# Kernel optimization log

Measured on AMD Instinct MI355X. Metric: run time of the kernel, lower is better.

Reference implementation:

```python
import jax, jax.numpy as jnp
import numpy as np

N_NEWS, N_ENT, N_TOP = 100000, 50000, 2000
D = 128
N_EDGES = 1600000
HID, OUT = 512, 128


def setup_inputs() -> dict:
    key = jax.random.key(0)
    ks = jax.random.split(key, 12)
    return {
        "news_feats": jax.random.normal(ks[0], (N_NEWS, D), jnp.float32),
        "entity_feats": jax.random.normal(ks[1], (N_ENT, D), jnp.float32),
        "topic_feats": jax.random.normal(ks[2], (N_TOP, D), jnp.float32),
        "ent_row": jax.random.randint(ks[3], (N_EDGES,), 0, N_NEWS, jnp.int32),
        "ent_col": jax.random.randint(ks[4], (N_EDGES,), 0, N_ENT, jnp.int32),
        "top_row": jax.random.randint(ks[5], (N_EDGES,), 0, N_NEWS, jnp.int32),
        "top_col": jax.random.randint(ks[6], (N_EDGES,), 0, N_TOP, jnp.int32),
        "W1": jax.random.normal(ks[7], (3 * D, HID), jnp.float32) * 0.05,
        "b1": jnp.zeros((HID,), jnp.float32),
        "W2": jax.random.normal(ks[8], (HID, OUT), jnp.float32) * 0.05,
        "b2": jnp.zeros((OUT,), jnp.float32),
    }


def _agg(feats, row, col, num_news):
    # SpMM with binary adjacency: sum neighbor feats per news node
    gathered = feats[col]                                   # [E, D]
    summed = jax.ops.segment_sum(gathered, row, num_segments=num_news)
    deg = jax.ops.segment_sum(jnp.ones_like(row, dtype=feats.dtype), row,
                              num_segments=num_news)
    return summed / (deg[:, None] + 1e-8)


def reference(news_feats, entity_feats, topic_feats, ent_row, ent_col,
              top_row, top_col, W1, b1, W2, b2):
    n = news_feats.shape[0]
    ent_agg = _agg(entity_feats, ent_row, ent_col, n)
    top_agg = _agg(topic_feats, top_row, top_col, n)
    out = jnp.concatenate([news_feats, ent_agg, top_agg], axis=1)  # [N, 3D]
    h = jnp.tanh(out @ W1 + b1)
    return h @ W2 + b2
```

## Files before the change

### kernel.cpp

```cpp
#include <hip/hip_runtime.h>
#include <hip/hip_bf16.h>

#define NN 100000
#define NE 50000
#define NT 2000
#define DD 128
#define NEDGE 1600000
#define HID 512
#define OUTD 128
#define K1 (3*DD)
#define NBKT 391

typedef __bf16 bf16x8 __attribute__((ext_vector_type(8)));
typedef __bf16 bf16x4 __attribute__((ext_vector_type(4)));
typedef float  f32x4  __attribute__((ext_vector_type(4)));

__device__ __forceinline__ __bf16 f2b(float f) {
    __hip_bfloat16 h = __float2bfloat16(f);
    union { __hip_bfloat16 h; __bf16 b; } u; u.h = h; return u.b;
}

__device__ __forceinline__ void gll16(const void* g, void* l) {
    __builtin_amdgcn_global_load_lds((const __attribute__((address_space(1))) void*)g,
                                     (__attribute__((address_space(3))) void*)l, 16, 0, 0);
}

__device__ __forceinline__ float ftanh(float x) {
    x = fminf(fmaxf(x, -15.f), 15.f);
    float t = __expf(2.f * x);
    return (t - 1.f) / (t + 1.f);
}

__global__ void conv_feats(const float* __restrict__ entf, const float* __restrict__ topf,
                           const float* __restrict__ news,
                           __bf16* __restrict__ entb, __bf16* __restrict__ topb,
                           __bf16* __restrict__ X) {
    long i = ((long)blockIdx.x * 256 + threadIdx.x) * 4;
    const long NEL = (long)NE * DD;
    const long NTL = (long)NT * DD;
    if (i < NEL) {
        float4 v = *(const float4*)(entf + i);
        *(bf16x4*)(entb + i) = bf16x4{f2b(v.x), f2b(v.y), f2b(v.z), f2b(v.w)};
    } else if (i < NEL + NTL) {
        long j = i - NEL;
        float4 v = *(const float4*)(topf + j);
        *(bf16x4*)(topb + j) = bf16x4{f2b(v.x), f2b(v.y), f2b(v.z), f2b(v.w)};
    } else {
        long j = i - NEL - NTL;
        long row = j >> 7, col = j & 127;
        float4 v = *(const float4*)(news + j);
        *(bf16x4*)(X + row * K1 + col) = bf16x4{f2b(v.x), f2b(v.y), f2b(v.z), f2b(v.w)};
    }
}

__global__ __launch_bounds__(256) void hist_buckets(const int* __restrict__ er,
                                                    const int* __restrict__ tr,
                                                    int* __restrict__ bc_e,
                                                    int* __restrict__ bc_t) {
    __shared__ int lhe[NBKT], lht[NBKT];
    const int tid = threadIdx.x;
    for (int i = tid; i < NBKT; i += 256) { lhe[i] = 0; lht[i] = 0; }
    __syncthreads();
    const int base = blockIdx.x * 8192;
    #pragma unroll 4
    for (int k = 0; k < 32; k++) {
        int e = base + k * 256 + tid;
        if (e < NEDGE) {
            atomicAdd(&lhe[er[e] >> 8], 1);
            atomicAdd(&lht[tr[e] >> 8], 1);
        }
    }
    __syncthreads();
    for (int i = tid; i < NBKT; i += 256) {
        if (lhe[i]) atomicAdd(&bc_e[i], lhe[i]);
        if (lht[i]) atomicAdd(&bc_t[i], lht[i]);
    }
}

__global__ void scan_buckets(int* __restrict__ bc_e, int* __restrict__ bc_t,
                             int* __restrict__ cur_e, int* __restrict__ cur_t,
                             int* __restrict__ offs_e, int* __restrict__ offs_t) {
    int* bc  = blockIdx.y ? bc_t : bc_e;
    int* cur = blockIdx.y ? cur_t : cur_e;
    int* offs = blockIdx.y ? offs_t : offs_e;
    __shared__ int s[512];
    int i = threadIdx.x;
    s[i] = (i < NBKT) ? bc[i] : 0;
    __syncthreads();
    #pragma unroll
    for (int off = 1; off < 512; off <<= 1) {
        int v = (i >= off) ? s[i - off] : 0;
        __syncthreads();
        s[i] += v;
        __syncthreads();
    }
    if (i < NBKT) {
        bc[i] = s[i];
        cur[i] = i ? s[i - 1] : 0;
    }
    if (i == 0) offs[0] = 0;
}

__global__ __launch_bounds__(256) void scatter_bucket(const int* __restrict__ er,
                                                      const int* __restrict__ ec,
                                                      const int* __restrict__ tr,
                                                      const int* __restrict__ tc,
                                                      int* __restrict__ cur_e,
                                                      int* __restrict__ cur_t,
                                                      int* __restrict__ be,
                                                      int* __restrict__ bt) {
    __shared__ int lhe[NBKT], lht[NBKT];
    __shared__ int lbe[NBKT], lbt[NBKT];
    const int tid = threadIdx.x;
    for (int i = tid; i < NBKT; i += 256) { lhe[i] = 0; lht[i] = 0; }
    __syncthreads();
    const int base = blockIdx.x * 4096;
    #pragma unroll 4
    for (int k = 0; k < 16; k++) {
        int e = base + k * 256 + tid;
        if (e < NEDGE) {
            atomicAdd(&lhe[er[e] >> 8], 1);
            atomicAdd(&lht[tr[e] >> 8], 1);
        }
    }
    __syncthreads();
    for (int i = tid; i < NBKT; i += 256) {
        int c = lhe[i];
        lbe[i] = c ? atomicAdd(&cur_e[i], c) : 0;
        lhe[i] = 0;
        c = lht[i];
        lbt[i] = c ? atomicAdd(&cur_t[i], c) : 0;
        lht[i] = 0;
    }
    __syncthreads();
    #pragma unroll 4
    for (int k = 0; k < 16; k++) {
        int e = base + k * 256 + tid;
        if (e < NEDGE) {
            int r = er[e];
            int b = r >> 8;
            int p = lbe[b] + atomicAdd(&lhe[b], 1);
            be[p] = ((r & 255) << 16) | ec[e];
            r = tr[e];
            b = r >> 8;
            p = lbt[b] + atomicAdd(&lht[b], 1);
            bt[p] = ((r & 255) << 16) | tc[e];
        }
    }
}

__global__ __launch_bounds__(256) void bucket_csr(const int* __restrict__ be,
                                                  const int* __restrict__ bt,
                                                  const int* __restrict__ bc_e,
                                                  const int* __restrict__ bc_t,
                                                  int* __restrict__ offs_e,
                                                  int* __restrict__ offs_t,
                                                  int* __restrict__ se,
                                                  int* __restrict__ st) {
    const int* buf = blockIdx.y ? bt : be;
    const int* bc  = blockIdx.y ? bc_t : bc_e;
    int* offs      = blockIdx.y ? offs_t : offs_e;
    int* sout      = blockIdx.y ? st : se;
    const int b = blockIdx.x;
    const int tid = threadIdx.x;
    const int start = b ? bc[b - 1] : 0;
    const int cnt = bc[b] - start;

    __shared__ int scn[256];
    __shared__ int lcur[256];
    scn[tid] = 0;
    __syncthreads();
    for (int i = tid; i < cnt; i += 256)
        atomicAdd(&scn[buf[start + i] >> 16], 1);
    __syncthreads();
    #pragma unroll
    for (int off = 1; off < 256; off <<= 1) {
        int v = (tid >= off) ? scn[tid - off] : 0;
        __syncthreads();
        scn[tid] += v;
        __syncthreads();
    }
    const int node = b * 256 + tid;
    if (node < NN) offs[node + 1] = start + scn[tid];
    lcur[tid] = start + (tid ? scn[tid - 1] : 0);
    __syncthreads();
    for (int i = tid; i < cnt; i += 256) {
        int v = buf[start + i];
        int p = atomicAdd(&lcur[v >> 16], 1);
        sout[p] = v & 0xFFFF;
    }
}

__global__ __launch_bounds__(256) void aggregate2(const __bf16* __restrict__ entb,
                                                  const __bf16* __restrict__ topb,
                                                  const int* __restrict__ offs_e,
                                                  const int* __restrict__ offs_t,
                                                  const int* __restrict__ se,
                                                  const int* __restrict__ st,
                                                  __bf16* __restrict__ X) {
    const int wave = threadIdx.x >> 6, lane = threadIdx.x & 63;
    const int node = blockIdx.x * 4 + wave;
    if (node >= NN) return;
    const int h = lane >> 4;
    const int d = (lane & 15) * 8;

    float ea[8] = {0,0,0,0,0,0,0,0};
    float pa[8] = {0,0,0,0,0,0,0,0};

    const int s0 = offs_e[node], s1 = offs_e[node + 1];
    int i = s0 + h;
    for (; i + 12 < s1; i += 16) {
        int c0 = se[i], c1 = se[i + 4], c2 = se[i + 8], c3 = se[i + 12];
        bf16x8 v0 = *(const bf16x8*)(entb + (long)c0 * DD + d);
        bf16x8 v1 = *(const bf16x8*)(entb + (long)c1 * DD + d);
        bf16x8 v2 = *(const bf16x8*)(entb + (long)c2 * DD + d);
        bf16x8 v3 = *(const bf16x8*)(entb + (long)c3 * DD + d);
        #pragma unroll
        for (int j = 0; j < 8; j++)
            ea[j] += ((float)v0[j] + (float)v1[j]) + ((float)v2[j] + (float)v3[j]);
    }
    for (; i < s1; i += 4) {
        bf16x8 v = *(const bf16x8*)(entb + (long)se[i] * DD + d);
        #pragma unroll
        for (int j = 0; j < 8; j++) ea[j] += (float)v[j];
    }

    const int t0 = offs_t[node], t1 = offs_t[node + 1];
    i = t0 + h;
    for (; i + 12 < t1; i += 16) {
        int c0 = st[i], c1 = st[i + 4], c2 = st[i + 8], c3 = st[i + 12];
        bf16x8 v0 = *(const bf16x8*)(topb + (long)c0 * DD + d);
        bf16x8 v1 = *(const bf16x8*)(topb + (long)c1 * DD + d);
        bf16x8 v2 = *(const bf16x8*)(topb + (long)c2 * DD + d);
        bf16x8 v3 = *(const bf16x8*)(topb + (long)c3 * DD + d);
        #pragma unroll
        for (int j = 0; j < 8; j++)
            pa[j] += ((float)v0[j] + (float)v1[j]) + ((float)v2[j] + (float)v3[j]);
    }
    for (; i < t1; i += 4) {
        bf16x8 v = *(const bf16x8*)(topb + (long)st[i] * DD + d);
        #pragma unroll
        for (int j = 0; j < 8; j++) pa[j] += (float)v[j];
    }

    #pragma unroll
    for (int j = 0; j < 8; j++) {
        ea[j] += __shfl_xor(ea[j], 16, 64);
        ea[j] += __shfl_xor(ea[j], 32, 64);
        pa[j] += __shfl_xor(pa[j], 16, 64);
        pa[j] += __shfl_xor(pa[j], 32, 64);
    }

    const float ie = 1.0f / ((float)(s1 - s0) + 1e-8f);
    const float it = 1.0f / ((float)(t1 - t0) + 1e-8f);
    __bf16* xr = X + (long)node * K1;
    if (h == 1) {
        *(bf16x8*)(xr + DD + d) = bf16x8{f2b(ea[0]*ie), f2b(ea[1]*ie), f2b(ea[2]*ie), f2b(ea[3]*ie),
                                         f2b(ea[4]*ie), f2b(ea[5]*ie), f2b(ea[6]*ie), f2b(ea[7]*ie)};
    } else if (h == 2) {
        *(bf16x8*)(xr + 2*DD + d) = bf16x8{f2b(pa[0]*it), f2b(pa[1]*it), f2b(pa[2]*it), f2b(pa[3]*it),
                                           f2b(pa[4]*it), f2b(pa[5]*it), f2b(pa[6]*it), f2b(pa[7]*it)};
    }
}

__global__ void conv_w(const float* __restrict__ W1, const float* __restrict__ W2,
                       __bf16* __restrict__ W1T, __bf16* __restrict__ W2T) {
    int i = blockIdx.x * 256 + threadIdx.x;
    if (i < K1 * HID) {
        int k = i / HID, n = i % HID;
        W1T[n * K1 + k] = f2b(W1[i]);
    } else {
        int j = i - K1 * HID;
        if (j < HID * OUTD) {
            int k = j / OUTD, n = j % OUTD;
            W2T[n * HID + k] = f2b(W2[j]);
        }
    }
}


__device__ __forceinline__ void stage_tile(const __bf16* __restrict__ src, int ldK,
                                           int k0, int row0, int rowmax,
                                           __bf16* lds, int w, int lane) {
    #pragma unroll
    for (int half = 0; half < 2; half++) {
        int ss = w * 64 + half * 256 + lane;
        int r = ss >> 2;
        int sw = (r & 3) ^ ((r >> 2) & 3);
        int c = (ss & 3) ^ sw;
        int gr = row0 + r; if (gr >= rowmax) gr = rowmax - 1;
        gll16(src + (long)gr * ldK + k0 + c * 8,
              lds + (w * 64 + half * 256) * 8);
    }
}

__device__ __forceinline__ bf16x8 frag(const __bf16* lds, int r, int q) {
    int sw = (r & 3) ^ ((r >> 2) & 3);
    return *(const bf16x8*)(lds + (r * 4 + (q ^ sw)) * 8);
}

__device__ __forceinline__ void hs_write(__bf16* Hs, int r, int c, __bf16 v) {
    int ch = c >> 3;
    int pch = ((((ch >> 2) ^ ((r >> 2) & 3)) << 2) | ((ch & 3) ^ (r & 3)));
    Hs[(r * 16 + pch) * 8 + (c & 7)] = v;
}
__device__ __forceinline__ bf16x8 hs_frag(const __bf16* Hs, int r, int kk, int q) {
    int pch = (((kk ^ ((r >> 2) & 3)) << 2) | (q ^ (r & 3)));
    return *(const bf16x8*)(Hs + (r * 16 + pch) * 8);
}

__global__ __launch_bounds__(256, 2) void mlp_fused(const __bf16* __restrict__ X,
                                                    const __bf16* __restrict__ W1T,
                                                    const float* __restrict__ b1,
                                                    const __bf16* __restrict__ W2T,
                                                    const float* __restrict__ b2,
                                                    float* __restrict__ out) {
    __shared__ __bf16 Xs[2][128 * 32];
    __shared__ __bf16 Ws[2][128 * 32];
    __shared__ __bf16 Hs[128 * 128];
    const int bm = blockIdx.x * 128;
    const int t = threadIdx.x;
    const int lane = t & 63;
    const int w = t >> 6;
    const int quad = lane >> 4;
    const int l16 = lane & 15;
    const int wm = w >> 1, wn = w & 1;

    f32x4 oacc[4][4];
    #pragma unroll
    for (int i = 0; i < 4; i++)
        #pragma unroll
        for (int j = 0; j < 4; j++)
            #pragma unroll
            for (int r = 0; r < 4; r++) oacc[i][j][r] = 0.0f;

    stage_tile(X,   K1, 0, bm, NN,  Xs[0], w, lane);
    stage_tile(W1T, K1, 0, 0,  HID, Ws[0], w, lane);
    int cur = 0;
    __syncthreads();

    for (int nc = 0; nc < 4; nc++) {
        f32x4 hacc[4][4];
        #pragma unroll
        for (int i = 0; i < 4; i++)
            #pragma unroll
            for (int j = 0; j < 4; j++)
                #pragma unroll
                for (int r = 0; r < 4; r++) hacc[i][j][r] = 0.0f;

        for (int kt = 0; kt < 12; kt++) {
            const int nb = cur ^ 1;
            if (kt < 11) {
                stage_tile(X,   K1, (kt + 1) * 32, bm,       NN,  Xs[nb], w, lane);
                stage_tile(W1T, K1, (kt + 1) * 32, nc * 128, HID, Ws[nb], w, lane);
            } else {
                stage_tile(W2T, HID, nc * 128, 0, OUTD, Ws[nb], w, lane);
            }
            bf16x8 af[4], bfr[4];
            #pragma unroll
            for (int i = 0; i < 4; i++) {
                af[i]  = frag(Xs[cur], wm * 64 + i * 16 + l16, quad);
                bfr[i] = frag(Ws[cur], wn * 64 + i * 16 + l16, quad);
            }
            __builtin_amdgcn_s_setprio(1);
            #pragma unroll
            for (int i = 0; i < 4; i++)
                #pragma unroll
                for (int j = 0; j < 4; j++)
                    hacc[i][j] = __builtin_amdgcn_mfma_f32_16x16x32_bf16(af[i], bfr[j], hacc[i][j], 0, 0, 0);
            __builtin_amdgcn_s_setprio(0);
            __syncthreads();
            cur = nb;
        }

        #pragma unroll
        for (int j = 0; j < 4; j++) {
            const int col = wn * 64 + j * 16 + l16;
            const float bb = b1[nc * 128 + col];
            #pragma unroll
            for (int i = 0; i < 4; i++) {
                const int rbase = wm * 64 + i * 16 + quad * 4;
                #pragma unroll
                for (int r = 0; r < 4; r++)
                    hs_write(Hs, rbase + r, col, f2b(ftanh(hacc[i][j][r] + bb)));
            }
        }
        __syncthreads();

        for (int kk = 0; kk < 4; kk++) {
            const int nb = cur ^ 1;
            if (kk < 3) {
                stage_tile(W2T, HID, nc * 128 + (kk + 1) * 32, 0, OUTD, Ws[nb], w, lane);
            } else if (nc < 3) {
                stage_tile(X,   K1, 0, bm,             NN,  Xs[nb], w, lane);
                stage_tile(W1T, K1, 0, (nc + 1) * 128, HID, Ws[nb], w, lane);
            }
            bf16x8 af[4], bfr[4];
            #pragma unroll
            for (int i = 0; i < 4; i++) {
                af[i]  = hs_frag(Hs, wm * 64 + i * 16 + l16, kk, quad);
                bfr[i] = frag(Ws[cur], wn * 64 + i * 16 + l16, quad);
            }
            __builtin_amdgcn_s_setprio(1);
            #pragma unroll
            for (int i = 0; i < 4; i++)
                #pragma unroll
                for (int j = 0; j < 4; j++)
                    oacc[i][j] = __builtin_amdgcn_mfma_f32_16x16x32_bf16(af[i], bfr[j], oacc[i][j], 0, 0, 0);
            __builtin_amdgcn_s_setprio(0);
            __syncthreads();
            cur = nb;
        }
    }

    float bb[4];
    #pragma unroll
    for (int j = 0; j < 4; j++) bb[j] = b2[wn * 64 + j * 16 + l16];
    #pragma unroll
    for (int i = 0; i < 4; i++) {
        #pragma unroll
        for (int r = 0; r < 4; r++) {
            const int gr = bm + wm * 64 + i * 16 + quad * 4 + r;
            if (gr < NN) {
                float* orow = out + (long)gr * OUTD + wn * 64 + l16;
                #pragma unroll
                for (int j = 0; j < 4; j++)
                    orow[j * 16] = oacc[i][j][r] + bb[j];
            }
        }
    }
}

extern "C" void kernel_launch(void* const* d_in, const int* in_sizes, int n_in,
                              void* d_out, int out_size, void* d_ws, size_t ws_size,
                              hipStream_t stream) {
    const float* news  = (const float*)d_in[0];
    const float* ent_f = (const float*)d_in[1];
    const float* top_f = (const float*)d_in[2];
    const int* ent_row = (const int*)d_in[3];
    const int* ent_col = (const int*)d_in[4];
    const int* top_row = (const int*)d_in[5];
    const int* top_col = (const int*)d_in[6];
    const float* W1 = (const float*)d_in[7];
    const float* b1 = (const float*)d_in[8];
    const float* W2 = (const float*)d_in[9];
    const float* b2 = (const float*)d_in[10];

    char* ws = (char*)d_ws;
    int* offs_e = (int*)(ws + 0);
    int* offs_t = (int*)(ws + 400016);
    int* bc_e   = (int*)(ws + 800032);
    int* bc_t   = (int*)(ws + 801596);
    int* cur_e  = (int*)(ws + 803160);
    int* cur_t  = (int*)(ws + 804724);
    int* be     = (int*)(ws + 806320);
    int* bt     = (int*)(ws + 7206320);
    int* se     = (int*)(ws + 13606320);
    int* st     = (int*)(ws + 20006320);
    __bf16* entb = (__bf16*)(ws + 26406336);
    __bf16* topb = (__bf16*)(ws + 39206336);
    __bf16* X   = (__bf16*)(ws + 102400000);
    __bf16* W1T = (__bf16*)(ws + 179200000);
    __bf16* W2T = (__bf16*)(ws + 179593216);

    hipMemsetAsync(ws + 800032, 0, 6256, stream);
    conv_w<<<1024, 256, 0, stream>>>(W1, W2, W1T, W2T);
    conv_feats<<<19000, 256, 0, stream>>>(ent_f, top_f, news, entb, topb, X);
    hist_buckets<<<196, 256, 0, stream>>>(ent_row, top_row, bc_e, bc_t);
    scan_buckets<<<dim3(1, 2), 512, 0, stream>>>(bc_e, bc_t, cur_e, cur_t, offs_e, offs_t);
    scatter_bucket<<<392, 256, 0, stream>>>(ent_row, ent_col, top_row, top_col,
                                            cur_e, cur_t, be, bt);
    bucket_csr<<<dim3(NBKT, 2), 256, 0, stream>>>(be, bt, bc_e, bc_t,
                                                  offs_e, offs_t, se, st);
    aggregate2<<<NN / 4, 256, 0, stream>>>(entb, topb, offs_e, offs_t, se, st, X);
    mlp_fused<<<782, 256, 0, stream>>>(X, W1T, b1, W2T, b2, (float*)d_out);
}
```

Before: 540.4 us.

## Triple-buffer LDS staging in fused MLP with vmcnt-based waits

Moves the fused MLP kernel from double-buffered to triple-buffered LDS tiles for X and W1. Loads are now issued two k-steps ahead, and explicit s_waitcnt vmcnt plus s_barrier replace the per-iteration __syncthreads. The W2 staging in the second GEMM ping-pongs between the spare third buffers, so the next chunk's first X/W1 tiles can be prefetched during the second GEMM. The goal is to hide global-load latency, at the cost of more LDS (which may cut occupancy below 2 blocks per CU) and fragile hand-counted vmcnt values.

New measurement: 528.2 us. 1.02x faster.

```diff
diff --git a/kernel.cpp b/kernel.cpp
--- a/kernel.cpp
+++ b/kernel.cpp
@@ -315,8 +315,8 @@
                                                     const __bf16* __restrict__ W2T,
                                                     const float* __restrict__ b2,
                                                     float* __restrict__ out) {
-    __shared__ __bf16 Xs[2][128 * 32];
-    __shared__ __bf16 Ws[2][128 * 32];
+    __shared__ __bf16 Xs[3][128 * 32];
+    __shared__ __bf16 Ws[3][128 * 32];
     __shared__ __bf16 Hs[128 * 128];
     const int bm = blockIdx.x * 128;
     const int t = threadIdx.x;
@@ -334,10 +334,10 @@
             #pragma unroll
             for (int r = 0; r < 4; r++) oacc[i][j][r] = 0.0f;
 
-    stage_tile(X,   K1, 0, bm, NN,  Xs[0], w, lane);
-    stage_tile(W1T, K1, 0, 0,  HID, Ws[0], w, lane);
-    int cur = 0;
-    __syncthreads();
+    stage_tile(X,   K1, 0,  bm, NN,  Xs[0], w, lane);
+    stage_tile(W1T, K1, 0,  0,  HID, Ws[0], w, lane);
+    stage_tile(X,   K1, 32, bm, NN,  Xs[1], w, lane);
+    stage_tile(W1T, K1, 32, 0,  HID, Ws[1], w, lane);
 
     for (int nc = 0; nc < 4; nc++) {
         f32x4 hacc[4][4];
@@ -348,19 +348,22 @@
                 #pragma unroll
                 for (int r = 0; r < 4; r++) hacc[i][j][r] = 0.0f;
 
+        #pragma unroll
         for (int kt = 0; kt < 12; kt++) {
-            const int nb = cur ^ 1;
-            if (kt < 11) {
-                stage_tile(X,   K1, (kt + 1) * 32, bm,       NN,  Xs[nb], w, lane);
-                stage_tile(W1T, K1, (kt + 1) * 32, nc * 128, HID, Ws[nb], w, lane);
-            } else {
-                stage_tile(W2T, HID, nc * 128, 0, OUTD, Ws[nb], w, lane);
-            }
+            const int cb = kt % 3;
+            if (kt < 11) asm volatile("s_waitcnt vmcnt(4)" ::: "memory");
+            else         asm volatile("s_waitcnt vmcnt(0)" ::: "memory");
+            __builtin_amdgcn_s_barrier();
             bf16x8 af[4], bfr[4];
             #pragma unroll
             for (int i = 0; i < 4; i++) {
-                af[i]  = frag(Xs[cur], wm * 64 + i * 16 + l16, quad);
-                bfr[i] = frag(Ws[cur], wn * 64 + i * 16 + l16, quad);
+                af[i]  = frag(Xs[cb], wm * 64 + i * 16 + l16, quad);
+                bfr[i] = frag(Ws[cb], wn * 64 + i * 16 + l16, quad);
+            }
+            if (kt < 10) {
+                const int nb = (kt + 2) % 3;
+                stage_tile(X,   K1, (kt + 2) * 32, bm,       NN,  Xs[nb], w, lane);
+                stage_tile(W1T, K1, (kt + 2) * 32, nc * 128, HID, Ws[nb], w, lane);
             }
             __builtin_amdgcn_s_setprio(1);
             #pragma unroll
@@ -369,9 +372,10 @@
                 for (int j = 0; j < 4; j++)
                     hacc[i][j] = __builtin_amdgcn_mfma_f32_16x16x32_bf16(af[i], bfr[j], hacc[i][j], 0, 0, 0);
             __builtin_amdgcn_s_setprio(0);
-            __syncthreads();
-            cur = nb;
-        }
+        }
+        __syncthreads();
+
+        stage_tile(W2T, HID, nc * 128, 0, OUTD, Ws[2], w, lane);
 
         #pragma unroll
         for (int j = 0; j < 4; j++) {
@@ -388,18 +392,24 @@
         __syncthreads();
 
         for (int kk = 0; kk < 4; kk++) {
-            const int nb = cur ^ 1;
-            if (kk < 3) {
-                stage_tile(W2T, HID, nc * 128 + (kk + 1) * 32, 0, OUTD, Ws[nb], w, lane);
-            } else if (nc < 3) {
-                stage_tile(X,   K1, 0, bm,             NN,  Xs[nb], w, lane);
-                stage_tile(W1T, K1, 0, (nc + 1) * 128, HID, Ws[nb], w, lane);
+            __bf16* curb = (kk & 1) ? Xs[2] : Ws[2];
+            __bf16* nxtb = (kk & 1) ? Ws[2] : Xs[2];
+            if (kk < 3)
+                stage_tile(W2T, HID, nc * 128 + (kk + 1) * 32, 0, OUTD, nxtb, w, lane);
+            if (nc < 3) {
+                if (kk == 2) {
+                    stage_tile(X,   K1, 0, bm,             NN,  Xs[0], w, lane);
+                    stage_tile(W1T, K1, 0, (nc + 1) * 128, HID, Ws[0], w, lane);
+                } else if (kk == 3) {
+                    stage_tile(X,   K1, 32, bm,             NN,  Xs[1], w, lane);
+                    stage_tile(W1T, K1, 32, (nc + 1) * 128, HID, Ws[1], w, lane);
+                }
             }
             bf16x8 af[4], bfr[4];
             #pragma unroll
             for (int i = 0; i < 4; i++) {
                 af[i]  = hs_frag(Hs, wm * 64 + i * 16 + l16, kk, quad);
-                bfr[i] = frag(Ws[cur], wn * 64 + i * 16 + l16, quad);
+                bfr[i] = frag(curb, wn * 64 + i * 16 + l16, quad);
             }
             __builtin_amdgcn_s_setprio(1);
             #pragma unroll
@@ -409,7 +419,6 @@
                     oacc[i][j] = __builtin_amdgcn_mfma_f32_16x16x32_bf16(af[i], bfr[j], oacc[i][j], 0, 0, 0);
             __builtin_amdgcn_s_setprio(0);
             __syncthreads();
-            cur = nb;
         }
     }
 
```

## Keep full X tile resident in LDS and triple-buffer weights with vmcnt-based pipelining

Applied to the files above, without the earlier changes.

The fused MLP kernel now stages the whole 128x384 X tile into LDS once, so the first hidden chunk loads it and the later chunks reuse it instead of reloading X from global memory. Weight tiles go through a 3-slot ring with prefetch two phases ahead, and the loop syncs with explicit vmcnt waits plus a single barrier instead of __syncthreads double-buffering. Bias values are also preloaded into registers. The larger LDS footprint (about 152KB) lowers occupancy to one block per CU, which reduces latency hiding across blocks.

New measurement: 536.0 us. Within noise of the previous version (-0.8%).

```diff
diff --git a/kernel.cpp b/kernel.cpp
--- a/kernel.cpp
+++ b/kernel.cpp
@@ -309,14 +309,29 @@
     return *(const bf16x8*)(Hs + (r * 16 + pch) * 8);
 }
 
-__global__ __launch_bounds__(256, 2) void mlp_fused(const __bf16* __restrict__ X,
+__device__ __forceinline__ void stage_for_phase(int g, int bm,
+        const __bf16* __restrict__ X, const __bf16* __restrict__ W1T,
+        const __bf16* __restrict__ W2T,
+        __bf16* Xs, __bf16* Wst, int w, int lane) {
+    if (g >= 64) return;
+    const int ncg = g >> 4, ph = g & 15;
+    __bf16* wb = Wst + (g % 3) * 4096;
+    if (ph < 12) {
+        if (ncg == 0) stage_tile(X, K1, ph * 32, bm, NN, Xs + ph * 4096, w, lane);
+        stage_tile(W1T, K1, ph * 32, ncg * 128, HID, wb, w, lane);
+    } else {
+        stage_tile(W2T, HID, ncg * 128 + (ph - 12) * 32, 0, OUTD, wb, w, lane);
+    }
+}
+
+__global__ __launch_bounds__(256, 1) void mlp_fused(const __bf16* __restrict__ X,
                                                     const __bf16* __restrict__ W1T,
                                                     const float* __restrict__ b1,
                                                     const __bf16* __restrict__ W2T,
                                                     const float* __restrict__ b2,
                                                     float* __restrict__ out) {
-    __shared__ __bf16 Xs[2][128 * 32];
-    __shared__ __bf16 Ws[2][128 * 32];
+    __shared__ __bf16 Xs[12 * 4096];
+    __shared__ __bf16 Wst[3 * 4096];
     __shared__ __bf16 Hs[128 * 128];
     const int bm = blockIdx.x * 128;
     const int t = threadIdx.x;
@@ -326,6 +341,16 @@
     const int l16 = lane & 15;
     const int wm = w >> 1, wn = w & 1;
 
+    float b1r[4][4], b2r[4];
+    #pragma unroll
+    for (int nc = 0; nc < 4; nc++)
+        #pragma unroll
+        for (int j = 0; j < 4; j++)
+            b1r[nc][j] = b1[nc * 128 + wn * 64 + j * 16 + l16];
+    #pragma unroll
+    for (int j = 0; j < 4; j++) b2r[j] = b2[wn * 64 + j * 16 + l16];
+    asm volatile("s_waitcnt vmcnt(0)" ::: "memory");
+
     f32x4 oacc[4][4];
     #pragma unroll
     for (int i = 0; i < 4; i++)
@@ -334,10 +359,8 @@
             #pragma unroll
             for (int r = 0; r < 4; r++) oacc[i][j][r] = 0.0f;
 
-    stage_tile(X,   K1, 0, bm, NN,  Xs[0], w, lane);
-    stage_tile(W1T, K1, 0, 0,  HID, Ws[0], w, lane);
-    int cur = 0;
-    __syncthreads();
+    stage_for_phase(0, bm, X, W1T, W2T, Xs, Wst, w, lane);
+    stage_for_phase(1, bm, X, W1T, W2T, Xs, Wst, w, lane);
 
     for (int nc = 0; nc < 4; nc++) {
         f32x4 hacc[4][4];
@@ -348,20 +371,20 @@
                 #pragma unroll
                 for (int r = 0; r < 4; r++) hacc[i][j][r] = 0.0f;
 
+        #pragma unroll
         for (int kt = 0; kt < 12; kt++) {
-            const int nb = cur ^ 1;
-            if (kt < 11) {
-                stage_tile(X,   K1, (kt + 1) * 32, bm,       NN,  Xs[nb], w, lane);
-                stage_tile(W1T, K1, (kt + 1) * 32, nc * 128, HID, Ws[nb], w, lane);
-            } else {
-                stage_tile(W2T, HID, nc * 128, 0, OUTD, Ws[nb], w, lane);
+            if (nc == 0 && kt <= 10) asm volatile("s_waitcnt vmcnt(4)" ::: "memory");
+            else                     asm volatile("s_waitcnt vmcnt(2)" ::: "memory");
+            __builtin_amdgcn_s_barrier();
+            const __bf16* xb = Xs + kt * 4096;
+            const __bf16* wb = Wst + ((nc * 16 + kt) % 3) * 4096;
+            bf16x8 af[4], bfr[4];
+            #pragma unroll
+            for (int i = 0; i < 4; i++) {
+                af[i]  = frag(xb, wm * 64 + i * 16 + l16, quad);
+                bfr[i] = frag(wb, wn * 64 + i * 16 + l16, quad);
             }
-            bf16x8 af[4], bfr[4];
-            #pragma unroll
-            for (int i = 0; i < 4; i++) {
-                af[i]  = frag(Xs[cur], wm * 64 + i * 16 + l16, quad);
-                bfr[i] = frag(Ws[cur], wn * 64 + i * 16 + l16, quad);
-            }
+            stage_for_phase(nc * 16 + kt + 2, bm, X, W1T, W2T, Xs, Wst, w, lane);
             __builtin_amdgcn_s_setprio(1);
             #pragma unroll
             for (int i = 0; i < 4; i++)
@@ -369,14 +392,12 @@
                 for (int j = 0; j < 4; j++)
                     hacc[i][j] = __builtin_amdgcn_mfma_f32_16x16x32_bf16(af[i], bfr[j], hacc[i][j], 0, 0, 0);
             __builtin_amdgcn_s_setprio(0);
-            __syncthreads();
-            cur = nb;
         }
 
         #pragma unroll
         for (int j = 0; j < 4; j++) {
             const int col = wn * 64 + j * 16 + l16;
-            const float bb = b1[nc * 128 + col];
+            const float bb = b1r[nc][j];
             #pragma unroll
             for (int i = 0; i < 4; i++) {
                 const int rbase = wm * 64 + i * 16 + quad * 4;
@@ -385,22 +406,22 @@
                     hs_write(Hs, rbase + r, col, f2b(ftanh(hacc[i][j][r] + bb)));
             }
         }
-        __syncthreads();
-
+        asm volatile("s_waitcnt lgkmcnt(0)" ::: "memory");
+        __builtin_amdgcn_s_barrier();
+
+        #pragma unroll
         for (int kk = 0; kk < 4; kk++) {
-            const int nb = cur ^ 1;
-            if (kk < 3) {
-                stage_tile(W2T, HID, nc * 128 + (kk + 1) * 32, 0, OUTD, Ws[nb], w, lane);
-            } else if (nc < 3) {
-                stage_tile(X,   K1, 0, bm,             NN,  Xs[nb], w, lane);
-                stage_tile(W1T, K1, 0, (nc + 1) * 128, HID, Ws[nb], w, lane);
-            }
+            if (nc == 3 && kk == 3) asm volatile("s_waitcnt vmcnt(0)" ::: "memory");
+            else                    asm volatile("s_waitcnt vmcnt(2)" ::: "memory");
+            __builtin_amdgcn_s_barrier();
+            const __bf16* wb = Wst + ((nc * 16 + 12 + kk) % 3) * 4096;
             bf16x8 af[4], bfr[4];
             #pragma unroll
             for (int i = 0; i < 4; i++) {
                 af[i]  = hs_frag(Hs, wm * 64 + i * 16 + l16, kk, quad);
-                bfr[i] = frag(Ws[cur], wn * 64 + i * 16 + l16, quad);
+                bfr[i] = frag(wb, wn * 64 + i * 16 + l16, quad);
             }
+            stage_for_phase(nc * 16 + 12 + kk + 2, bm, X, W1T, W2T, Xs, Wst, w, lane);
             __builtin_amdgcn_s_setprio(1);
             #pragma unroll
             for (int i = 0; i < 4; i++)
@@ -408,14 +429,9 @@
                 for (int j = 0; j < 4; j++)
                     oacc[i][j] = __builtin_amdgcn_mfma_f32_16x16x32_bf16(af[i], bfr[j], oacc[i][j], 0, 0, 0);
             __builtin_amdgcn_s_setprio(0);
-            __syncthreads();
-            cur = nb;
-        }
-    }
-
-    float bb[4];
-    #pragma unroll
-    for (int j = 0; j < 4; j++) bb[j] = b2[wn * 64 + j * 16 + l16];
+        }
+    }
+
     #pragma unroll
     for (int i = 0; i < 4; i++) {
         #pragma unroll
@@ -425,7 +441,7 @@
                 float* orow = out + (long)gr * OUTD + wn * 64 + l16;
                 #pragma unroll
                 for (int j = 0; j < 4; j++)
-                    orow[j * 16] = oacc[i][j][r] + bb[j];
+                    orow[j * 16] = oacc[i][j][r] + b2r[j];
             }
         }
     }
```
